# Optimization experiments

Hardware: AMD Instinct MI355X
Metric: run time of the kernel (lower is better)

Reference implementation:

```python
import jax, jax.numpy as jnp
import numpy as np

VOCAB, EMB, HID, LABELS = 50000, 300, 200, 10
B, S = 32, 512


def _gru_direction(emb, h0, w_ih, w_hh, b_ih, b_hh):
    """Run a GRUCell recurrence over time. emb: [B,S,E], h0: [B,H] -> [B,S,H].
    PyTorch GRUCell gate order: r, z, n."""
    # Precompute input projections for all timesteps (one big GEMM).
    gi = jnp.einsum('bse,ge->bsg', emb, w_ih) + b_ih  # [B,S,3H]
    gi = jnp.transpose(gi, (1, 0, 2))  # [S,B,3H] for scan
    H = h0.shape[-1]

    def step(h, gi_t):
        gh = h @ w_hh.T + b_hh  # [B,3H]
        i_r, i_z, i_n = gi_t[:, :H], gi_t[:, H:2 * H], gi_t[:, 2 * H:]
        h_r, h_z, h_n = gh[:, :H], gh[:, H:2 * H], gh[:, 2 * H:]
        r = jax.nn.sigmoid(i_r + h_r)
        z = jax.nn.sigmoid(i_z + h_z)
        n = jnp.tanh(i_n + r * h_n)
        h_new = (1.0 - z) * n + z * h
        return h_new, h_new

    _, hs = jax.lax.scan(step, h0, gi)  # hs: [S,B,H]
    return jnp.transpose(hs, (1, 0, 2))  # [B,S,H]


def setup_inputs() -> dict:
    key = jax.random.key(0)
    ks = jax.random.split(key, 14)
    sc = 0.05
    return {
        'text': jax.random.randint(ks[0], (B, S), 0, VOCAB),
        'embedding': jax.random.normal(ks[1], (VOCAB, EMB), jnp.float32) * sc,
        'w_ih_f': jax.random.normal(ks[2], (3 * HID, EMB), jnp.float32) * sc,
        'w_hh_f': jax.random.normal(ks[3], (3 * HID, HID), jnp.float32) * sc,
        'b_ih_f': jax.random.normal(ks[4], (3 * HID,), jnp.float32) * sc,
        'b_hh_f': jax.random.normal(ks[5], (3 * HID,), jnp.float32) * sc,
        'w_ih_b': jax.random.normal(ks[6], (3 * HID, EMB), jnp.float32) * sc,
        'w_hh_b': jax.random.normal(ks[7], (3 * HID, HID), jnp.float32) * sc,
        'b_ih_b': jax.random.normal(ks[8], (3 * HID,), jnp.float32) * sc,
        'b_hh_b': jax.random.normal(ks[9], (3 * HID,), jnp.float32) * sc,
        'lin_w': jax.random.normal(ks[10], (LABELS, 2 * HID), jnp.float32) * sc,
        'lin_b': jax.random.normal(ks[11], (LABELS,), jnp.float32) * sc,
        'h0_f': jax.random.uniform(ks[12], (B, HID), jnp.float32),
        'h0_b': jax.random.uniform(ks[13], (B, HID), jnp.float32),
    }


def reference(text, embedding, w_ih_f, w_hh_f, b_ih_f, b_hh_f,
              w_ih_b, w_hh_b, b_ih_b, b_hh_b, lin_w, lin_b, h0_f, h0_b):
    emb = embedding[text]  # [B,S,E]
    hid = w_hh_f.shape[-1]
    h0f = (h0_f - 0.5) / hid  # matches (rand-0.5)/hidden_unit
    h0b = (h0_b - 0.5) / hid
    out_f = _gru_direction(emb, h0f, w_ih_f, w_hh_f, b_ih_f, b_hh_f)
    # backward direction: iterate t = S-1 .. 0, outputs re-ordered to time order
    out_b = _gru_direction(emb[:, ::-1, :], h0b, w_ih_b, w_hh_b, b_ih_b, b_hh_b)[:, ::-1, :]
    out = jnp.concatenate([out_f, out_b], axis=2)  # [B,S,2H]
    preds = out @ lin_w.T + lin_b  # [B,S,LABELS]
    return preds
```

## Files before the change

kernel.cpp:

```cpp
#include <hip/hip_runtime.h>
#include <hip/hip_fp16.h>

typedef _Float16 h8 __attribute__((ext_vector_type(8)));
typedef _Float16 h4 __attribute__((ext_vector_type(4)));
typedef _Float16 h2 __attribute__((ext_vector_type(2)));
typedef float f4 __attribute__((ext_vector_type(4)));

#define EMB    300
#define HID    200
#define NR     600
#define GIS    1200
#define SEQ    512
#define MTOT   16384
#define WROW_N 240000
#define WROW_P 240032

#if defined(__has_builtin)
#if __has_builtin(__builtin_amdgcn_fdot2)
#define USE_FDOT2 1
#endif
#endif

__device__ __forceinline__ float fdot2f(h2 a, h2 b, float c) {
#ifdef USE_FDOT2
  return __builtin_amdgcn_fdot2(a, b, c, false);
#else
  return c + (float)a[0] * (float)b[0] + (float)a[1] * (float)b[1];
#endif
}

__device__ __forceinline__ float sigm(float x) { return 1.0f / (1.0f + __expf(-x)); }
__device__ __forceinline__ float tanhf_(float x) { return 1.0f - 2.0f / (1.0f + __expf(2.0f * x)); }

__device__ __forceinline__ float qsum(float x) {
  x += __int_as_float(__builtin_amdgcn_mov_dpp(__float_as_int(x), 0xB1, 0xF, 0xF, true));
  x += __int_as_float(__builtin_amdgcn_mov_dpp(__float_as_int(x), 0x4E, 0xF, 0xF, true));
  return x;
}

__global__ __launch_bounds__(256) void prep_kernel(
    const float* __restrict__ w_ih_f, const float* __restrict__ w_ih_b,
    const float* __restrict__ b_ih_f, const float* __restrict__ b_ih_b,
    const float* __restrict__ w_hh_f, const float* __restrict__ w_hh_b,
    _Float16* __restrict__ Wfrag, float* __restrict__ bias_cat,
    _Float16* __restrict__ Wrow) {
  int idx = blockIdx.x * 256 + threadIdx.x;
  if (idx < 76 * 10 * 64 * 8) {
    int e = idx & 7, f = idx >> 3;
    int lane = f & 63; f >>= 6;
    int ks = f % 10, nt = f / 10;
    int n = nt * 16 + (lane & 15);
    int k = ks * 32 + (lane >> 4) * 8 + e;
    float v = 0.0f;
    if (k < EMB) {
      if (n < NR) v = w_ih_f[n * EMB + k];
      else if (n < 2 * NR) v = w_ih_b[(n - NR) * EMB + k];
    }
    Wfrag[idx] = (_Float16)v;
  }
  if (idx < 1216) {
    float bv = 0.0f;
    if (idx < NR) bv = b_ih_f[idx];
    else if (idx < 2 * NR) bv = b_ih_b[idx - NR];
    bias_cat[idx] = bv;
  }
  if (idx < WROW_P) {
    float v = 0.0f;
    if (idx < WROW_N) {
      int d = idx / 120000, rem = idx - d * 120000;
      v = (d ? w_hh_b : w_hh_f)[rem];
    }
    Wrow[idx] = (_Float16)v;
  }
}

__global__ __launch_bounds__(512) void gi_gemm(
    const int* __restrict__ text, const float* __restrict__ emb,
    const _Float16* __restrict__ Wfrag, const float* __restrict__ bias_cat,
    __half* __restrict__ gi) {
  __shared__ _Float16 At[128][328];
  const int t = threadIdx.x;
  const int m0 = blockIdx.x * 128;
  {
    const int row = t >> 2;
    const int q = t & 3;
    const int tokid = text[m0 + row];
    const float4* ep = (const float4*)(emb + (size_t)tokid * EMB);
    for (int c4 = q; c4 < 75; c4 += 4) {
      float4 v = ep[c4];
      h4 hv = { (_Float16)v.x, (_Float16)v.y, (_Float16)v.z, (_Float16)v.w };
      *(h4*)&At[row][c4 * 4] = hv;
    }
    for (int c = 300 + q; c < 328; c += 4) At[row][c] = (_Float16)0.0f;
  }
  __syncthreads();

  const int wv = t >> 6, lane = t & 63;
  const int l15 = lane & 15, l4 = lane >> 4;
  const int nhalf = wv >> 2;
  const int ms0 = (wv & 3) * 2;
  const int r0 = ms0 * 16 + l15;
  const int r1 = r0 + 16;

  for (int c2 = 0; c2 < 2; ++c2) {
    const int nbase = nhalf * 38 + c2 * 19;
    f4 acc0[19], acc1[19];
#pragma unroll
    for (int i = 0; i < 19; ++i) { acc0[i] = (f4){0,0,0,0}; acc1[i] = (f4){0,0,0,0}; }
    for (int ks = 0; ks < 10; ++ks) {
      h8 a0 = *(const h8*)&At[r0][ks * 32 + l4 * 8];
      h8 a1 = *(const h8*)&At[r1][ks * 32 + l4 * 8];
#pragma unroll
      for (int i = 0; i < 19; ++i) {
        h8 bf = ((const h8*)Wfrag)[((size_t)(nbase + i) * 10 + ks) * 64 + lane];
        acc0[i] = __builtin_amdgcn_mfma_f32_16x16x32_f16(a0, bf, acc0[i], 0, 0, 0);
        acc1[i] = __builtin_amdgcn_mfma_f32_16x16x32_f16(a1, bf, acc1[i], 0, 0, 0);
      }
    }
#pragma unroll
    for (int i = 0; i < 19; ++i) {
      const int n = (nbase + i) * 16 + l15;
      if (n < GIS) {
        const float bv = bias_cat[n];
#pragma unroll
        for (int j = 0; j < 4; ++j) {
          const int mA = m0 + ms0 * 16 + l4 * 4 + j;
          gi[(size_t)mA * GIS + n] = (__half)(acc0[i][j] + bv);
          gi[(size_t)(mA + 16) * GIS + n] = (__half)(acc1[i][j] + bv);
        }
      }
    }
  }
}

#define DOT8(w, x, A, B)                                        \
  A = fdot2f((h2){(w)[0],(w)[1]}, (h2){(x)[0],(x)[1]}, A);      \
  B = fdot2f((h2){(w)[2],(w)[3]}, (h2){(x)[2],(x)[3]}, B);      \
  A = fdot2f((h2){(w)[4],(w)[5]}, (h2){(x)[4],(x)[5]}, A);      \
  B = fdot2f((h2){(w)[6],(w)[7]}, (h2){(x)[6],(x)[7]}, B);

#define ROW_VARS(i) h8 w##i##0, w##i##1, w##i##2, w##i##3, w##i##4, w##i##5, w##i##6
#define ROW_LOAD(i) do { const h8* p = (const h8*)(Wrow + wbase + (size_t)(i) * 200); \
  w##i##0 = p[0]; w##i##1 = p[1]; w##i##2 = p[2]; w##i##3 = p[3];                     \
  w##i##4 = p[4]; w##i##5 = p[5]; w##i##6 = p[6]; } while (0)
#define ROW_DOT(i, A, B) do {                                   \
  DOT8(w##i##0, x0, A, B); DOT8(w##i##1, x1, A, B);             \
  DOT8(w##i##2, x2, A, B); DOT8(w##i##3, x3, A, B);             \
  DOT8(w##i##4, x4, A, B); DOT8(w##i##5, x5, A, B);             \
  DOT8(w##i##6, x6, A, B); } while (0)

__global__ __launch_bounds__(512, 1) void gru_rec(
    const _Float16* __restrict__ Wrow,
    const float* __restrict__ b_hh_f, const float* __restrict__ b_hh_b,
    const float* __restrict__ h0_f,  const float* __restrict__ h0_b,
    const __half* __restrict__ gi, __half* __restrict__ hs) {
  const int t = threadIdx.x;
  const int dir = blockIdx.x >> 5;
  const int b = blockIdx.x & 31;
  const float* bhh_g = dir ? b_hh_b : b_hh_f;
  const float* h0 = dir ? h0_b : h0_f;

  __shared__ __align__(16) _Float16 h_sh[224];
  __shared__ float y_lds[NR];
  __shared__ __align__(16) _Float16 gi_lds[2][608];

  const int rg = t >> 2, kq = t & 3;
  const bool arow = (rg < 120);
  const int rbase = arow ? rg * 5 : 0;
  const size_t wbase = (size_t)dir * 120000 + (size_t)rbase * 200 + 56 * kq;

  ROW_VARS(0); ROW_VARS(1); ROW_VARS(2); ROW_VARS(3); ROW_VARS(4);
  ROW_LOAD(0); ROW_LOAD(1); ROW_LOAD(2); ROW_LOAD(3); ROW_LOAD(4);

  float bb0 = 0, bb1 = 0, bb2 = 0, hreg = 0;
  if (t < HID) {
    bb0 = bhh_g[t]; bb1 = bhh_g[200 + t]; bb2 = bhh_g[400 + t];
    hreg = (h0[b * HID + t] - 0.5f) * (1.0f / (float)HID);
  }
  if (t < 224) h_sh[t] = (t < HID) ? (_Float16)hreg : (_Float16)0.0f;
  {
    const int s0 = dir ? (SEQ - 1) : 0;
    const h4* g0 = (const h4*)(gi + (size_t)(b * SEQ + s0) * GIS + dir * NR);
    if (t < 150) ((h4*)gi_lds[0])[t] = g0[t];
  }
  __syncthreads();

  const h8* hh = (const h8*)&h_sh[56 * kq];

  for (int st = 0; st < SEQ; ++st) {
    const int cur = st & 1, nxt = cur ^ 1;
    const int s = dir ? (SEQ - 1 - st) : st;
    h4 pf = (h4){(_Float16)0, (_Float16)0, (_Float16)0, (_Float16)0};
    const bool do_pf = (t < 150) && (st < SEQ - 1);
    if (do_pf) {
      const int sn = dir ? (SEQ - 2 - st) : (st + 1);
      pf = ((const h4*)(gi + (size_t)(b * SEQ + sn) * GIS + dir * NR))[t];
    }
    h8 x0 = hh[0], x1 = hh[1], x2 = hh[2], x3 = hh[3], x4 = hh[4], x5 = hh[5], x6 = hh[6];
    float a0A = 0, a0B = 0, a1A = 0, a1B = 0, a2A = 0, a2B = 0,
          a3A = 0, a3B = 0, a4A = 0, a4B = 0;
    ROW_DOT(0, a0A, a0B); ROW_DOT(1, a1A, a1B); ROW_DOT(2, a2A, a2B);
    ROW_DOT(3, a3A, a3B); ROW_DOT(4, a4A, a4B);
    const float s0 = qsum(a0A + a0B), s1 = qsum(a1A + a1B), s2 = qsum(a2A + a2B),
                s3 = qsum(a3A + a3B), s4 = qsum(a4A + a4B);
    if (arow) {
      y_lds[rbase + kq] = (kq == 0) ? s0 : (kq == 1) ? s1 : (kq == 2) ? s2 : s3;
      if (kq == 0) y_lds[rbase + 4] = s4;
    }
    __syncthreads();
    if (t < HID) {
      const _Float16* gih = gi_lds[cur];
      const float ir = (float)gih[t];
      const float iz = (float)gih[200 + t];
      const float inn = (float)gih[400 + t];
      const float rgt = sigm(ir + y_lds[t] + bb0);
      const float zg = sigm(iz + y_lds[200 + t] + bb1);
      const float ng = tanhf_(inn + rgt * (y_lds[400 + t] + bb2));
      hreg = (1.0f - zg) * ng + zg * hreg;
      h_sh[t] = (_Float16)hreg;
      hs[(size_t)(b * SEQ + s) * 400 + dir * HID + t] = (__half)hreg;
    }
    if (do_pf) ((h4*)gi_lds[nxt])[t] = pf;
    __syncthreads();
  }
}

__global__ __launch_bounds__(256) void final_linear(
    const __half* __restrict__ hs, const float* __restrict__ lin_w,
    const float* __restrict__ lin_b, float* __restrict__ out) {
  __shared__ _Float16 hsl[64][400];
  __shared__ _Float16 lwl[10][400];
  const int t = threadIdx.x;
  const int m0 = blockIdx.x * 64;
  const ushort4* hp = (const ushort4*)(hs + (size_t)m0 * 400);
  for (int idx = t; idx < 64 * 100; idx += 256) {
    ushort4 v = hp[idx];
    const int row = idx / 100, c = idx - row * 100;
    *(ushort4*)&hsl[row][c * 4] = v;
  }
  for (int idx = t; idx < 10 * 400; idx += 256) {
    (&lwl[0][0])[idx] = (_Float16)lin_w[idx];
  }
  __syncthreads();
  for (int idx = t; idx < 640; idx += 256) {
    const int m = idx / 10, c = idx - (idx / 10) * 10;
    const h2* hr = (const h2*)hsl[m];
    const h2* wr = (const h2*)lwl[c];
    float acc = 0.0f;
#pragma unroll 8
    for (int kk = 0; kk < 200; ++kk) acc = fdot2f(hr[kk], wr[kk], acc);
    out[(size_t)(m0 + m) * 10 + c] = acc + lin_b[c];
  }
}

extern "C" void kernel_launch(void* const* d_in, const int* in_sizes, int n_in,
                              void* d_out, int out_size, void* d_ws, size_t ws_size,
                              hipStream_t stream) {
  const int*   text   = (const int*)d_in[0];
  const float* emb    = (const float*)d_in[1];
  const float* w_ih_f = (const float*)d_in[2];
  const float* w_hh_f = (const float*)d_in[3];
  const float* b_ih_f = (const float*)d_in[4];
  const float* b_hh_f = (const float*)d_in[5];
  const float* w_ih_b = (const float*)d_in[6];
  const float* w_hh_b = (const float*)d_in[7];
  const float* b_ih_b = (const float*)d_in[8];
  const float* b_hh_b = (const float*)d_in[9];
  const float* lin_w  = (const float*)d_in[10];
  const float* lin_b  = (const float*)d_in[11];
  const float* h0_f   = (const float*)d_in[12];
  const float* h0_b   = (const float*)d_in[13];
  float* out = (float*)d_out;

  char* ws = (char*)d_ws;
  _Float16* Wfrag    = (_Float16*)(ws);
  float*    bias_cat = (float*)(ws + 778240);
  __half*   gi       = (__half*)(ws + 783360);
  _Float16* Wrow     = (_Float16*)(ws + 40104960);
  __half*   hs       = (__half*)(ws + 40585088);

  prep_kernel<<<dim3(1520), dim3(256), 0, stream>>>(
      w_ih_f, w_ih_b, b_ih_f, b_ih_b, w_hh_f, w_hh_b, Wfrag, bias_cat, Wrow);
  gi_gemm<<<dim3(MTOT / 128), dim3(512), 0, stream>>>(
      text, emb, Wfrag, bias_cat, gi);
  gru_rec<<<dim3(64), dim3(512), 0, stream>>>(
      Wrow, b_hh_f, b_hh_b, h0_f, h0_b, gi, hs);
  final_linear<<<dim3(MTOT / 64), dim3(256), 0, stream>>>(
      hs, lin_w, lin_b, out);
}
```

Baseline: 726.0 us.

## Keep recurrent weights partly in LDS instead of registers, rest from global

The GRU recurrence kernel stops holding its five W_hh rows per thread in registers. It copies the first 380 rows (about 152KB) into dynamic LDS and reads them from there at every timestep, while the remaining rows are re-read from global/L2 each step. This frees a large register footprint, and launch_bounds no longer forces one block per CU. The cost is extra LDS and global load traffic on the serial critical path of each of the 512 steps.

Result: slower. 1.460 ms (+101.1%).

```diff
diff --git a/kernel.cpp b/kernel.cpp
--- a/kernel.cpp
+++ b/kernel.cpp
@@ -14,6 +14,14 @@
 #define MTOT   16384
 #define WROW_N 240000
 #define WROW_P 240032
+
+#define LGRP    76
+#define LROWS   (LGRP * 5)
+#define WLDS_B  (LROWS * 200 * 2)
+#define HSH_OFF WLDS_B
+#define Y_OFF   (HSH_OFF + 448)
+#define GI_OFF  (Y_OFF + 2400)
+#define LDS_TOT (GI_OFF + 2432)
 
 #if defined(__has_builtin)
 #if __has_builtin(__builtin_amdgcn_fdot2)
@@ -139,38 +147,38 @@
   A = fdot2f((h2){(w)[4],(w)[5]}, (h2){(x)[4],(x)[5]}, A);      \
   B = fdot2f((h2){(w)[6],(w)[7]}, (h2){(x)[6],(x)[7]}, B);
 
-#define ROW_VARS(i) h8 w##i##0, w##i##1, w##i##2, w##i##3, w##i##4, w##i##5, w##i##6
-#define ROW_LOAD(i) do { const h8* p = (const h8*)(Wrow + wbase + (size_t)(i) * 200); \
-  w##i##0 = p[0]; w##i##1 = p[1]; w##i##2 = p[2]; w##i##3 = p[3];                     \
-  w##i##4 = p[4]; w##i##5 = p[5]; w##i##6 = p[6]; } while (0)
-#define ROW_DOT(i, A, B) do {                                   \
-  DOT8(w##i##0, x0, A, B); DOT8(w##i##1, x1, A, B);             \
-  DOT8(w##i##2, x2, A, B); DOT8(w##i##3, x3, A, B);             \
-  DOT8(w##i##4, x4, A, B); DOT8(w##i##5, x5, A, B);             \
-  DOT8(w##i##6, x6, A, B); } while (0)
-
-__global__ __launch_bounds__(512, 1) void gru_rec(
+#define ROW_DOTP(P, A, B) do {                                   \
+    const h8* rp_ = (const h8*)(P);                              \
+    h8 w0_ = rp_[0], w1_ = rp_[1], w2_ = rp_[2], w3_ = rp_[3],   \
+       w4_ = rp_[4], w5_ = rp_[5], w6_ = rp_[6];                 \
+    DOT8(w0_, x0, A, B); DOT8(w1_, x1, A, B); DOT8(w2_, x2, A, B); \
+    DOT8(w3_, x3, A, B); DOT8(w4_, x4, A, B); DOT8(w5_, x5, A, B); \
+    DOT8(w6_, x6, A, B); } while (0)
+
+__global__ __launch_bounds__(512) void gru_rec(
     const _Float16* __restrict__ Wrow,
     const float* __restrict__ b_hh_f, const float* __restrict__ b_hh_b,
     const float* __restrict__ h0_f,  const float* __restrict__ h0_b,
     const __half* __restrict__ gi, __half* __restrict__ hs) {
+  extern __shared__ __align__(16) char smem[];
+  _Float16* wlds   = (_Float16*)smem;
+  _Float16* h_sh   = (_Float16*)(smem + HSH_OFF);
+  float*    y_lds  = (float*)(smem + Y_OFF);
+  _Float16* gi_lds = (_Float16*)(smem + GI_OFF);
+
   const int t = threadIdx.x;
   const int dir = blockIdx.x >> 5;
   const int b = blockIdx.x & 31;
   const float* bhh_g = dir ? b_hh_b : b_hh_f;
   const float* h0 = dir ? h0_b : h0_f;
 
-  __shared__ __align__(16) _Float16 h_sh[224];
-  __shared__ float y_lds[NR];
-  __shared__ __align__(16) _Float16 gi_lds[2][608];
-
   const int rg = t >> 2, kq = t & 3;
   const bool arow = (rg < 120);
   const int rbase = arow ? rg * 5 : 0;
-  const size_t wbase = (size_t)dir * 120000 + (size_t)rbase * 200 + 56 * kq;
-
-  ROW_VARS(0); ROW_VARS(1); ROW_VARS(2); ROW_VARS(3); ROW_VARS(4);
-  ROW_LOAD(0); ROW_LOAD(1); ROW_LOAD(2); ROW_LOAD(3); ROW_LOAD(4);
+  const _Float16* Wd = Wrow + (size_t)dir * 120000;
+
+  for (int i = t; i < WLDS_B / 16; i += 512)
+    ((f4*)wlds)[i] = ((const f4*)Wd)[i];
 
   float bb0 = 0, bb1 = 0, bb2 = 0, hreg = 0;
   if (t < HID) {
@@ -181,10 +189,12 @@
   {
     const int s0 = dir ? (SEQ - 1) : 0;
     const h4* g0 = (const h4*)(gi + (size_t)(b * SEQ + s0) * GIS + dir * NR);
-    if (t < 150) ((h4*)gi_lds[0])[t] = g0[t];
+    if (t < 150) ((h4*)gi_lds)[t] = g0[t];
   }
   __syncthreads();
 
+  const _Float16* wl = wlds + rbase * 200 + 56 * kq;
+  const _Float16* wg = Wd + (size_t)rbase * 200 + 56 * kq;
   const h8* hh = (const h8*)&h_sh[56 * kq];
 
   for (int st = 0; st < SEQ; ++st) {
@@ -199,8 +209,19 @@
     h8 x0 = hh[0], x1 = hh[1], x2 = hh[2], x3 = hh[3], x4 = hh[4], x5 = hh[5], x6 = hh[6];
     float a0A = 0, a0B = 0, a1A = 0, a1B = 0, a2A = 0, a2B = 0,
           a3A = 0, a3B = 0, a4A = 0, a4B = 0;
-    ROW_DOT(0, a0A, a0B); ROW_DOT(1, a1A, a1B); ROW_DOT(2, a2A, a2B);
-    ROW_DOT(3, a3A, a3B); ROW_DOT(4, a4A, a4B);
+    if (rg < LGRP) {
+      ROW_DOTP(wl +   0, a0A, a0B);
+      ROW_DOTP(wl + 200, a1A, a1B);
+      ROW_DOTP(wl + 400, a2A, a2B);
+      ROW_DOTP(wl + 600, a3A, a3B);
+      ROW_DOTP(wl + 800, a4A, a4B);
+    } else if (arow) {
+      ROW_DOTP(wg +   0, a0A, a0B);
+      ROW_DOTP(wg + 200, a1A, a1B);
+      ROW_DOTP(wg + 400, a2A, a2B);
+      ROW_DOTP(wg + 600, a3A, a3B);
+      ROW_DOTP(wg + 800, a4A, a4B);
+    }
     const float s0 = qsum(a0A + a0B), s1 = qsum(a1A + a1B), s2 = qsum(a2A + a2B),
                 s3 = qsum(a3A + a3B), s4 = qsum(a4A + a4B);
     if (arow) {
@@ -209,7 +230,7 @@
     }
     __syncthreads();
     if (t < HID) {
-      const _Float16* gih = gi_lds[cur];
+      const _Float16* gih = gi_lds + cur * 608;
       const float ir = (float)gih[t];
       const float iz = (float)gih[200 + t];
       const float inn = (float)gih[400 + t];
@@ -220,7 +241,7 @@
       h_sh[t] = (_Float16)hreg;
       hs[(size_t)(b * SEQ + s) * 400 + dir * HID + t] = (__half)hreg;
     }
-    if (do_pf) ((h4*)gi_lds[nxt])[t] = pf;
+    if (do_pf) ((h4*)(gi_lds + nxt * 608))[t] = pf;
     __syncthreads();
   }
 }
@@ -279,11 +300,16 @@
   _Float16* Wrow     = (_Float16*)(ws + 40104960);
   __half*   hs       = (__half*)(ws + 40585088);
 
+  static int lds_attr_set = 0;
+  hipFuncSetAttribute((const void*)gru_rec,
+                      hipFuncAttributeMaxDynamicSharedMemorySize, LDS_TOT);
+  (void)lds_attr_set;
+
   prep_kernel<<<dim3(1520), dim3(256), 0, stream>>>(
       w_ih_f, w_ih_b, b_ih_f, b_ih_b, w_hh_f, w_hh_b, Wfrag, bias_cat, Wrow);
   gi_gemm<<<dim3(MTOT / 128), dim3(512), 0, stream>>>(
       text, emb, Wfrag, bias_cat, gi);
-  gru_rec<<<dim3(64), dim3(512), 0, stream>>>(
+  gru_rec<<<dim3(64), dim3(512), LDS_TOT, stream>>>(
       Wrow, b_hh_f, b_hh_b, h0_f, h0_b, gi, hs);
   final_linear<<<dim3(MTOT / 64), dim3(256), 0, stream>>>(
       hs, lin_w, lin_b, out);
```
